# Performance work log

Hardware: AMD Instinct MI355X
Metric: run time of the kernel (lower is better)

Reference implementation:

```python
import jax, jax.numpy as jnp
import numpy as np

HEADS = 16
DIM_HEAD = 64
SCALE = DIM_HEAD ** -0.5


def setup_inputs() -> dict:
    key = jax.random.key(0)
    ks = jax.random.split(key, 5)
    B, N, D = 2, 2048, 1024  # query_dim = inner_dim = 1024
    s = 0.02
    return {
        "x": jax.random.normal(ks[0], (B, N, D), dtype=jnp.float32),
        "Wq": jax.random.normal(ks[1], (D, D), dtype=jnp.float32) * s,
        "Wk": jax.random.normal(ks[2], (D, D), dtype=jnp.float32) * s,
        "Wv": jax.random.normal(ks[3], (D, D), dtype=jnp.float32) * s,
        "Wout": jax.random.normal(ks[4], (D, D), dtype=jnp.float32) * s,
        "bout": jnp.zeros((D,), dtype=jnp.float32),
    }


def reference(x, Wq, Wk, Wv, Wout, bout):
    B, N, D = x.shape
    h, dh = HEADS, DIM_HEAD
    # projections (torch Linear: y = x @ W.T); context = x (self-attention)
    q = (x @ Wq.T).reshape(B, N, h, dh).transpose(0, 2, 1, 3)  # b h n d
    k = (x @ Wk.T).reshape(B, N, h, dh).transpose(0, 2, 1, 3)
    v = (x @ Wv.T).reshape(B, N, h, dh).transpose(0, 2, 1, 3)
    # scaled dot-product attention; chunk loop in original is math-equivalent
    s = jnp.einsum('bhid,bhjd->bhij', q, k) * SCALE
    p = jax.nn.softmax(s, axis=-1)
    o = jnp.einsum('bhij,bhjd->bhid', p, v)  # b h n d
    o = o.transpose(0, 2, 1, 3).reshape(B, N, h * dh)
    return o @ Wout.T + bout
```

## Files before the change

### kernel.cpp

```cpp
#include <hip/hip_runtime.h>
#include <stdint.h>

using bf16x8 = __attribute__((ext_vector_type(8))) short;
using f32x4  = __attribute__((ext_vector_type(4))) float;
using s16x4  = __attribute__((ext_vector_type(4))) short;

__device__ __forceinline__ short f2bf(float f) {
    union { float f; uint32_t u; } v; v.f = f;
    uint32_t u = v.u;
    uint32_t r = (u + 0x7fffu + ((u >> 16) & 1u)) >> 16;
    return (short)r;
}

__device__ __forceinline__ uint32_t cvtpk_bf16(float a, float b) {
    uint32_t r;
    asm("v_cvt_pk_bf16_f32 %0, %1, %2" : "=v"(r) : "v"(a), "v"(b));
    return r;
}

__device__ __forceinline__ void gload_lds16(const void* g, void* l) {
    __builtin_amdgcn_global_load_lds(
        reinterpret_cast<const uint32_t __attribute__((address_space(1)))*>(
            reinterpret_cast<uintptr_t>(g)),
        reinterpret_cast<uint32_t __attribute__((address_space(3)))*>(
            reinterpret_cast<uintptr_t>(l)),
        16, 0, 0);
}

__global__ __launch_bounds__(256) void cvt_all(
    const float* __restrict__ x, const float* __restrict__ wq,
    const float* __restrict__ wk, const float* __restrict__ wv,
    const float* __restrict__ wo,
    short* __restrict__ xb, short* __restrict__ wqb, short* __restrict__ wkb,
    short* __restrict__ wvb, short* __restrict__ wob)
{
    int i = blockIdx.x * 256 + threadIdx.x;
    const float* src; short* dst; int off;
    if      (i < 1048576) { src = x;  dst = xb;  off = i; }
    else if (i < 1310720) { src = wq; dst = wqb; off = i - 1048576; }
    else if (i < 1572864) { src = wk; dst = wkb; off = i - 1310720; }
    else if (i < 1835008) { src = wv; dst = wvb; off = i - 1572864; }
    else                  { src = wo; dst = wob; off = i - 1835008; }
    float4 f = ((const float4*)src)[off];
    s16x4 r; r[0] = f2bf(f.x); r[1] = f2bf(f.y); r[2] = f2bf(f.z); r[3] = f2bf(f.w);
    ((s16x4*)dst)[off] = r;
}

template <bool IS_OUT>
__global__ __launch_bounds__(256) void gemm_bt(
    const short* __restrict__ A,
    const short* __restrict__ Bq, const short* __restrict__ Bk,
    const short* __restrict__ Bv,
    short* __restrict__ qb, short* __restrict__ kb, short* __restrict__ vtb,
    float* __restrict__ outp, const float* __restrict__ bias)
{
    constexpr int BN = IS_OUT ? 64 : 128;
    constexpr int BC = BN / 32;
    constexpr int NI = BN / 32;
    __shared__ short As[2][128 * 64];
    __shared__ short Bs[2][BN * 64];
    const int tid  = threadIdx.x;
    const int wave = tid >> 6, lane = tid & 63;
    const int lo = lane & 15, hi = lane >> 4;

    const int nwg = gridDim.x * gridDim.y * gridDim.z;
    int lin = blockIdx.x + blockIdx.y * gridDim.x +
              blockIdx.z * gridDim.x * gridDim.y;
    const int s = (lin & 7) * (nwg >> 3) + (lin >> 3);
    const int m_base = IS_OUT ? ((s >> 4) & 31) * 128 : ((s >> 3) & 31) * 128;
    const int n_base = IS_OUT ? (s & 15) * 64        : (s & 7) * 128;
    const int z = IS_OUT ? 0 : (s >> 8);

    const short* Bw = IS_OUT ? Bq : (z == 0 ? Bq : (z == 1 ? Bk : Bv));
    const int wr = wave >> 1, wc = wave & 1;

    f32x4 acc[4][NI];
#pragma unroll
    for (int i = 0; i < 4; ++i)
#pragma unroll
        for (int j = 0; j < NI; ++j) acc[i][j] = (f32x4){0.f, 0.f, 0.f, 0.f};

    const int se = (lane & 7) * 8;
    const short* Ag = A  + (size_t)(m_base + wave * 32 + (lane >> 3)) * 1024 + se;
    const short* Bg = Bw + (size_t)(n_base + wave * (BN / 4) + (lane >> 3)) * 1024 + se;

    auto GSTAGE = [&](int kt) {
        const int k0 = kt * 64, bf = kt & 1;
#pragma unroll
        for (int c = 0; c < 4; ++c)
            gload_lds16(Ag + (size_t)c * 8 * 1024 + k0, &As[bf][(wave * 32 + c * 8) * 64]);
#pragma unroll
        for (int c = 0; c < BC; ++c)
            gload_lds16(Bg + (size_t)c * 8 * 1024 + k0,
                        &Bs[bf][(wave * (BN / 4) + c * 8) * 64]);
    };

    GSTAGE(0);
    for (int kt = 0; kt < 16; ++kt) {
        if (kt < 15) {
            GSTAGE(kt + 1);
            if constexpr (IS_OUT)
                asm volatile("s_waitcnt vmcnt(6)" ::: "memory");
            else
                asm volatile("s_waitcnt vmcnt(8)" ::: "memory");
        } else {
            asm volatile("s_waitcnt vmcnt(0)" ::: "memory");
        }
        __builtin_amdgcn_s_barrier();
        const int bf = kt & 1;
#pragma unroll
        for (int ks = 0; ks < 2; ++ks) {
            bf16x8 av[4], bv[NI];
#pragma unroll
            for (int i = 0; i < 4; ++i)
                av[i] = *(const bf16x8*)&As[bf][(wr * 64 + i * 16 + lo) * 64 + ks * 32 + hi * 8];
#pragma unroll
            for (int i = 0; i < NI; ++i)
                bv[i] = *(const bf16x8*)&Bs[bf][(wc * (BN / 2) + i * 16 + lo) * 64 + ks * 32 + hi * 8];
#pragma unroll
            for (int mi = 0; mi < 4; ++mi)
#pragma unroll
                for (int ni = 0; ni < NI; ++ni)
                    acc[mi][ni] = __builtin_amdgcn_mfma_f32_16x16x32_bf16(
                        av[mi], bv[ni], acc[mi][ni], 0, 0, 0);
        }
        asm volatile("s_waitcnt lgkmcnt(0)" ::: "memory");
        __builtin_amdgcn_s_barrier();
    }

#pragma unroll
    for (int mi = 0; mi < 4; ++mi) {
#pragma unroll
        for (int ni = 0; ni < NI; ++ni) {
            const int n = n_base + wc * (BN / 2) + ni * 16 + lo;
            if (IS_OUT) {
                const float bsv = bias[n];
#pragma unroll
                for (int i = 0; i < 4; ++i) {
                    const int m = m_base + wr * 64 + mi * 16 + hi * 4 + i;
                    outp[(size_t)m * 1024 + n] = acc[mi][ni][i] + bsv;
                }
            } else {
                const int h = n >> 6, d = n & 63;
                if (z == 2) {
                    const int m0 = m_base + wr * 64 + mi * 16 + hi * 4;
                    const int b = m0 >> 11, ns = m0 & 2047;
                    s16x4 pk;
#pragma unroll
                    for (int i = 0; i < 4; ++i) pk[i] = f2bf(acc[mi][ni][i]);
                    *(s16x4*)&vtb[(((size_t)b * 16 + h) * 64 + d) * 2048 + ns] = pk;
                } else {
                    short* dstp = (z == 0) ? qb : kb;
                    const float scl = (z == 0) ? 0.18033688011112042f : 1.0f;
#pragma unroll
                    for (int i = 0; i < 4; ++i) {
                        const int m = m_base + wr * 64 + mi * 16 + hi * 4 + i;
                        const int b = m >> 11, ns = m & 2047;
                        dstp[(((size_t)b * 16 + h) * 2048 + ns) * 64 + d] =
                            f2bf(acc[mi][ni][i] * scl);
                    }
                }
            }
        }
    }
}


#define QKT16_(TT, S) do {                                                     \
    const char* kb_ = (const char*)K_lds[(TT) % 3];                            \
    bf16x8 kf_[4];                                                             \
    _Pragma("unroll")                                                          \
    for (int mi = 0; mi < 4; ++mi)                                             \
        kf_[mi] = *(const bf16x8*)(kb_ + (mi * 16 + lo) * 128 +                \
                                   ((hi ^ (lo & 7)) << 4));                    \
    _Pragma("unroll")                                                          \
    for (int mi = 0; mi < 4; ++mi)                                             \
        _Pragma("unroll")                                                      \
        for (int nf = 0; nf < 2; ++nf)                                         \
            S[mi][nf] = __builtin_amdgcn_mfma_f32_16x16x32_bf16(               \
                kf_[mi], qf[nf][0], Z4, 0, 0, 0);                              \
    _Pragma("unroll")                                                          \
    for (int mi = 0; mi < 4; ++mi)                                             \
        kf_[mi] = *(const bf16x8*)(kb_ + (mi * 16 + lo) * 128 +                \
                                   (((4 + hi) ^ (lo & 7)) << 4));              \
    _Pragma("unroll")                                                          \
    for (int mi = 0; mi < 4; ++mi)                                             \
        _Pragma("unroll")                                                      \
        for (int nf = 0; nf < 2; ++nf)                                         \
            S[mi][nf] = __builtin_amdgcn_mfma_f32_16x16x32_bf16(               \
                kf_[mi], qf[nf][1], S[mi][nf], 0, 0, 0);                       \
    } while (0)

#define HALF16_(T, SC, SN, DOQ) do {                                           \
    if ((T) < 30) {                                                            \
        STAGE((T) + 2);                                                        \
        asm volatile("s_waitcnt vmcnt(4)" ::: "memory");                       \
    } else {                                                                   \
        asm volatile("s_waitcnt vmcnt(0)" ::: "memory");                       \
    }                                                                          \
    __builtin_amdgcn_s_barrier();                                              \
    if (DOQ) {                                                                 \
        __builtin_amdgcn_s_setprio(1);                                         \
        QKT16_((T) + 1, SN);                                                   \
        __builtin_amdgcn_s_setprio(0);                                         \
    }                                                                          \
                          \
    float pm_[2];                                                              \
    _Pragma("unroll")                                                          \
    for (int nf = 0; nf < 2; ++nf) {                                           \
        float a0 = fmaxf(fmaxf(SC[0][nf][0], SC[0][nf][1]),                    \
                         fmaxf(SC[0][nf][2], SC[0][nf][3]));                   \
        float a1 = fmaxf(fmaxf(SC[1][nf][0], SC[1][nf][1]),                    \
                         fmaxf(SC[1][nf][2], SC[1][nf][3]));                   \
        float a2 = fmaxf(fmaxf(SC[2][nf][0], SC[2][nf][1]),                    \
                         fmaxf(SC[2][nf][2], SC[2][nf][3]));                   \
        float a3 = fmaxf(fmaxf(SC[3][nf][0], SC[3][nf][1]),                    \
                         fmaxf(SC[3][nf][2], SC[3][nf][3]));                   \
        pm_[nf] = fmaxf(fmaxf(a0, a1), fmaxf(a2, a3));                         \
    }                                                                          \
    const int keep_ = (pm_[0] <= mrow[0] + 8.f) && (pm_[1] <= mrow[1] + 8.f);  \
    if (!__all(keep_)) {                  \
        float alpha_[2];                                                       \
        _Pragma("unroll")                                                      \
        for (int nf = 0; nf < 2; ++nf) {                                       \
            float m4 = pm_[nf];                                                \
            m4 = fmaxf(m4, __shfl_xor(m4, 16));                                \
            m4 = fmaxf(m4, __shfl_xor(m4, 32));                                \
            const float mn = fmaxf(mrow[nf], m4);                              \
            alpha_[nf] = __builtin_amdgcn_exp2f(mrow[nf] - mn);                \
            mrow[nf]  = mn;                                                    \
            lrow[nf] *= alpha_[nf];                                            \
        }                                                                      \
        _Pragma("unroll")                                                      \
        for (int mi = 0; mi < 2; ++mi)                                         \
            _Pragma("unroll")                                                  \
            for (int i = 0; i < 4; ++i) {                                      \
                const float av = __shfl(alpha_[mi], hi * 4 + i);               \
                _Pragma("unroll")                                              \
                for (int nf = 0; nf < 4; ++nf) oacc[mi][nf][i] *= av;          \
            }                                                                  \
    }                                                                          \
    _Pragma("unroll")                                                          \
    for (int nf = 0; nf < 2; ++nf) {        \
        float s0 = 0.f, s1 = 0.f, s2 = 0.f, s3 = 0.f;                          \
        _Pragma("unroll")                                                      \
        for (int mi = 0; mi < 4; ++mi) {                                       \
            SC[mi][nf][0] = __builtin_amdgcn_exp2f(SC[mi][nf][0] - mrow[nf]);  \
            s0 += SC[mi][nf][0];                                               \
            SC[mi][nf][1] = __builtin_amdgcn_exp2f(SC[mi][nf][1] - mrow[nf]);  \
            s1 += SC[mi][nf][1];                                               \
            SC[mi][nf][2] = __builtin_amdgcn_exp2f(SC[mi][nf][2] - mrow[nf]);  \
            s2 += SC[mi][nf][2];                                               \
            SC[mi][nf][3] = __builtin_amdgcn_exp2f(SC[mi][nf][3] - mrow[nf]);  \
            s3 += SC[mi][nf][3];                                               \
        }                                                                      \
        lrow[nf] += (s0 + s1) + (s2 + s3);                                     \
    }                                                                          \
                 \
    _Pragma("unroll")                                                          \
    for (int nf = 0; nf < 2; ++nf)                                             \
        _Pragma("unroll")                                                      \
        for (int mi = 0; mi < 4; ++mi) {                                       \
            uint2 w;                                                           \
            w.x = cvtpk_bf16(SC[mi][nf][0], SC[mi][nf][1]);                    \
            w.y = cvtpk_bf16(SC[mi][nf][2], SC[mi][nf][3]);                    \
            const int row  = nf * 16 + lo;                                     \
            const int slot = (mi * 2 + (hi >> 1)) ^ (lo & 7);                  \
            *(uint2*)(pbase + row * 128 + (slot << 4) + (hi & 1) * 8) = w;     \
        }                                                                      \
    asm volatile("s_waitcnt lgkmcnt(0)" ::: "memory");                         \
    __builtin_amdgcn_sched_barrier(0);                                         \
           \
    __builtin_amdgcn_s_setprio(1);                                             \
    _Pragma("unroll")                                                          \
    for (int ks = 0; ks < 2; ++ks) {                                           \
        bf16x8 pa_[2], vf_[4];                                                 \
        _Pragma("unroll")                                                      \
        for (int mi = 0; mi < 2; ++mi)                                         \
            pa_[mi] = *(const bf16x8*)(pbase + (mi * 16 + lo) * 128 +          \
                                       (((ks * 4 + hi) ^ (lo & 7)) << 4));     \
        _Pragma("unroll")                                                      \
        for (int nf = 0; nf < 4; ++nf)                                         \
            vf_[nf] = *(const bf16x8*)((const char*)V_lds[(T) % 3] +           \
                                       (nf * 16 + lo) * 128 +                  \
                                       (((ks * 4 + hi) ^ (lo & 7)) << 4));     \
        _Pragma("unroll")                                                      \
        for (int mi = 0; mi < 2; ++mi)                                         \
            _Pragma("unroll")                                                  \
            for (int nf = 0; nf < 4; ++nf)                                     \
                oacc[mi][nf] = __builtin_amdgcn_mfma_f32_16x16x32_bf16(        \
                    pa_[mi], vf_[nf], oacc[mi][nf], 0, 0, 0);                  \
    }                                                                          \
    __builtin_amdgcn_s_setprio(0);                                             \
    asm volatile("s_waitcnt lgkmcnt(0)" ::: "memory");                         \
    __builtin_amdgcn_s_barrier();                                              \
    } while (0)

__global__ __launch_bounds__(256) void attn(
    const short* __restrict__ qg, const short* __restrict__ kg,
    const short* __restrict__ vtg, short* __restrict__ ob)
{
    __shared__ short K_lds[3][64 * 64];
    __shared__ short V_lds[3][64 * 64];
    __shared__ short P_lds[4 * 32 * 64];

    const int tid  = threadIdx.x;
    const int wave = tid >> 6, lane = tid & 63;
    const int lo = lane & 15, hi = lane >> 4;

    int bid = blockIdx.y * 16 + blockIdx.x;
    bid = (bid & 7) * 64 + (bid >> 3);
    const int bh = bid >> 4;
    const int qw = (bid & 15) * 128 + wave * 32;

    bf16x8 qf[2][2];
#pragma unroll
    for (int nf = 0; nf < 2; ++nf)
#pragma unroll
        for (int ks = 0; ks < 2; ++ks)
            qf[nf][ks] = *(const bf16x8*)&qg[((size_t)bh * 2048 + qw + nf * 16 + lo) * 64 +
                                             ks * 32 + hi * 8];
    asm volatile("s_waitcnt vmcnt(0)" ::: "memory");

    f32x4 oacc[2][4];
#pragma unroll
    for (int mi = 0; mi < 2; ++mi)
#pragma unroll
        for (int nf = 0; nf < 4; ++nf) oacc[mi][nf] = (f32x4){0.f, 0.f, 0.f, 0.f};
    float mrow[2] = {-1e30f, -1e30f};
    float lrow[2] = {0.f, 0.f};
    const f32x4 Z4 = (f32x4){0.f, 0.f, 0.f, 0.f};

    char* pbase = (char*)P_lds + wave * 4096;
    const short* kgb = kg  + (size_t)bh * 2048 * 64;
    const short* vgb = vtg + (size_t)bh * 64 * 2048;

    const int stV = wave >> 1, rbase = (wave & 1) * 32;
    auto STAGE = [&](int t) {
        const int buf = t % 3, kv0 = t * 64;
#pragma unroll
        for (int c = 0; c < 4; ++c) {
            const int r  = rbase + c * 8 + (lane >> 3);
            const int sg = (lane & 7) ^ (r & 7);
            if (stV == 0)
                gload_lds16(kgb + (size_t)(kv0 + r) * 64 + sg * 8,
                            &K_lds[buf][(rbase + c * 8) * 64]);
            else
                gload_lds16(vgb + (size_t)r * 2048 + kv0 + sg * 8,
                            &V_lds[buf][(rbase + c * 8) * 64]);
        }
    };

    STAGE(0); STAGE(1);

    f32x4 sA[4][2], sB[4][2];

    asm volatile("s_waitcnt vmcnt(4)" ::: "memory");
    __builtin_amdgcn_s_barrier();
    QKT16_(0, sA);

    for (int u = 0; u < 15; ++u) {
        HALF16_(2 * u,     sA, sB, 1);
        HALF16_(2 * u + 1, sB, sA, 1);
    }
    HALF16_(30, sA, sB, 1);
    HALF16_(31, sB, sA, 0);

    float lfull[2];
#pragma unroll
    for (int nf = 0; nf < 2; ++nf) {
        float ts = lrow[nf];
        ts += __shfl_xor(ts, 16);
        ts += __shfl_xor(ts, 32);
        lfull[nf] = ts;
    }
    const int b = bh >> 4, h = bh & 15;
#pragma unroll
    for (int mi = 0; mi < 2; ++mi)
#pragma unroll
        for (int i = 0; i < 4; ++i) {
            const float lv = __shfl(lfull[mi], hi * 4 + i);
            const float r  = 1.0f / lv;
            const int qrow = qw + mi * 16 + hi * 4 + i;
#pragma unroll
            for (int nf = 0; nf < 4; ++nf)
                ob[((size_t)b * 2048 + qrow) * 1024 + h * 64 + nf * 16 + lo] =
                    f2bf(oacc[mi][nf][i] * r);
        }
}

extern "C" void kernel_launch(void* const* d_in, const int* in_sizes, int n_in,
                              void* d_out, int out_size, void* d_ws, size_t ws_size,
                              hipStream_t stream) {
    const float* x   = (const float*)d_in[0];
    const float* Wq  = (const float*)d_in[1];
    const float* Wk  = (const float*)d_in[2];
    const float* Wv  = (const float*)d_in[3];
    const float* Wo  = (const float*)d_in[4];
    const float* bo  = (const float*)d_in[5];
    float* outp = (float*)d_out;

    char* ws = (char*)d_ws;
    short* xb  = (short*)(ws);
    short* qb  = (short*)(ws + (8u  << 20));
    short* kb  = (short*)(ws + (16u << 20));
    short* vtb = (short*)(ws + (24u << 20));
    short* ob  = (short*)(ws + (32u << 20));
    short* wqb = (short*)(ws + (40u << 20));
    short* wkb = (short*)(ws + (42u << 20));
    short* wvb = (short*)(ws + (44u << 20));
    short* wob = (short*)(ws + (46u << 20));

    cvt_all<<<8192, 256, 0, stream>>>(x, Wq, Wk, Wv, Wo, xb, wqb, wkb, wvb, wob);
    gemm_bt<false><<<dim3(8, 32, 3), 256, 0, stream>>>(
        xb, wqb, wkb, wvb, qb, kb, vtb, nullptr, nullptr);
    attn<<<dim3(16, 32), 256, 0, stream>>>(qb, kb, vtb, ob);
    gemm_bt<true><<<dim3(16, 32, 1), 256, 0, stream>>>(
        ob, wob, nullptr, nullptr, nullptr, nullptr, nullptr, outp, bo);
}
```

Before: 128.7 us.

## Feed softmax P to PV MFMA from registers via permuted V layout

Removes the per-wave P shared-memory round trip (LDS write, waitcnt, LDS read) by packing the softmax probabilities directly from the QK^T accumulator registers into MFMA A operands. To make the register layout match the MFMA k-ordering, the V projection epilogue now writes V^T with a permuted sequence index within each 64-element block. This also frees 16KB of LDS per block, which may allow more occupancy, but ties the V layout to this specific MFMA register mapping.

```diff
diff --git a/kernel.cpp b/kernel.cpp
--- a/kernel.cpp
+++ b/kernel.cpp
@@ -145,10 +145,13 @@
                 if (z == 2) {
                     const int m0 = m_base + wr * 64 + mi * 16 + hi * 4;
                     const int b = m0 >> 11, ns = m0 & 2047;
+                    const int k6 = ns & 63;
+                    const int nsp = (ns & ~63) | (k6 & 0x20) |
+                                    ((k6 & 0x10) >> 2) | ((k6 & 0x0C) << 1);
                     s16x4 pk;
 #pragma unroll
                     for (int i = 0; i < 4; ++i) pk[i] = f2bf(acc[mi][ni][i]);
-                    *(s16x4*)&vtb[(((size_t)b * 16 + h) * 64 + d) * 2048 + ns] = pk;
+                    *(s16x4*)&vtb[(((size_t)b * 16 + h) * 64 + d) * 2048 + nsp] = pk;
                 } else {
                     short* dstp = (z == 0) ? qb : kb;
                     const float scl = (z == 0) ? 0.18033688011112042f : 1.0f;
@@ -257,39 +260,34 @@
         lrow[nf] += (s0 + s1) + (s2 + s3);                                     \
     }                                                                          \
                  \
-    _Pragma("unroll")                                                          \
-    for (int nf = 0; nf < 2; ++nf)                                             \
-        _Pragma("unroll")                                                      \
-        for (int mi = 0; mi < 4; ++mi) {                                       \
-            uint2 w;                                                           \
-            w.x = cvtpk_bf16(SC[mi][nf][0], SC[mi][nf][1]);                    \
-            w.y = cvtpk_bf16(SC[mi][nf][2], SC[mi][nf][3]);                    \
-            const int row  = nf * 16 + lo;                                     \
-            const int slot = (mi * 2 + (hi >> 1)) ^ (lo & 7);                  \
-            *(uint2*)(pbase + row * 128 + (slot << 4) + (hi & 1) * 8) = w;     \
+    uint32_t W2_[4][2][2];                                                     \
+    _Pragma("unroll")                                                          \
+    for (int mi = 0; mi < 4; ++mi)                                             \
+        _Pragma("unroll")                                                      \
+        for (int nf = 0; nf < 2; ++nf) {                                       \
+            W2_[mi][nf][0] = cvtpk_bf16(SC[mi][nf][0], SC[mi][nf][1]);         \
+            W2_[mi][nf][1] = cvtpk_bf16(SC[mi][nf][2], SC[mi][nf][3]);         \
         }                                                                      \
-    asm volatile("s_waitcnt lgkmcnt(0)" ::: "memory");                         \
-    __builtin_amdgcn_sched_barrier(0);                                         \
            \
     __builtin_amdgcn_s_setprio(1);                                             \
     _Pragma("unroll")                                                          \
     for (int ks = 0; ks < 2; ++ks) {                                           \
-        bf16x8 pa_[2], vf_[4];                                                 \
-        _Pragma("unroll")                                                      \
-        for (int mi = 0; mi < 2; ++mi)                                         \
-            pa_[mi] = *(const bf16x8*)(pbase + (mi * 16 + lo) * 128 +          \
-                                       (((ks * 4 + hi) ^ (lo & 7)) << 4));     \
+        bf16x8 vf_[4];                                                         \
         _Pragma("unroll")                                                      \
         for (int nf = 0; nf < 4; ++nf)                                         \
             vf_[nf] = *(const bf16x8*)((const char*)V_lds[(T) % 3] +           \
                                        (nf * 16 + lo) * 128 +                  \
                                        (((ks * 4 + hi) ^ (lo & 7)) << 4));     \
         _Pragma("unroll")                                                      \
-        for (int mi = 0; mi < 2; ++mi)                                         \
+        for (int mo = 0; mo < 2; ++mo) {                                       \
+            union { uint32_t u[4]; bf16x8 v; } pk_;                            \
+            pk_.u[0] = W2_[ks * 2][mo][0];     pk_.u[1] = W2_[ks * 2][mo][1];  \
+            pk_.u[2] = W2_[ks * 2 + 1][mo][0]; pk_.u[3] = W2_[ks * 2 + 1][mo][1]; \
             _Pragma("unroll")                                                  \
             for (int nf = 0; nf < 4; ++nf)                                     \
-                oacc[mi][nf] = __builtin_amdgcn_mfma_f32_16x16x32_bf16(        \
-                    pa_[mi], vf_[nf], oacc[mi][nf], 0, 0, 0);                  \
+                oacc[mo][nf] = __builtin_amdgcn_mfma_f32_16x16x32_bf16(        \
+                    pk_.v, vf_[nf], oacc[mo][nf], 0, 0, 0);                    \
+        }                                                                      \
     }                                                                          \
     __builtin_amdgcn_s_setprio(0);                                             \
     asm volatile("s_waitcnt lgkmcnt(0)" ::: "memory");                         \
@@ -302,7 +300,6 @@
 {
     __shared__ short K_lds[3][64 * 64];
     __shared__ short V_lds[3][64 * 64];
-    __shared__ short P_lds[4 * 32 * 64];
 
     const int tid  = threadIdx.x;
     const int wave = tid >> 6, lane = tid & 63;
@@ -331,7 +328,6 @@
     float lrow[2] = {0.f, 0.f};
     const f32x4 Z4 = (f32x4){0.f, 0.f, 0.f, 0.f};
 
-    char* pbase = (char*)P_lds + wave * 4096;
     const short* kgb = kg  + (size_t)bh * 2048 * 64;
     const short* vgb = vtg + (size_t)bh * 64 * 2048;
 
```

Measured after the change: 128.0 us. No clear change (-0.5%).
